# Performance work log

Hardware: AMD Instinct MI355X
Metric: run time of the kernel (lower is better)

The kernel has to match this reference:

```python
import jax, jax.numpy as jnp
import numpy as np

B, S, D = 4, 4096, 2048
E, H, SPE = 64, 1024, 1
NUM_SLOTS = E * SPE
TEMP = 1.0


def setup_inputs() -> dict:
    key = jax.random.key(0)
    ks = jax.random.split(key, 6)
    x = jax.random.normal(ks[0], (B, S, D), dtype=jnp.float32)
    W_disp = jax.random.normal(ks[1], (NUM_SLOTS, D), dtype=jnp.float32) * 0.02
    # torch Linear default init ~ U(-1/sqrt(fan_in), 1/sqrt(fan_in))
    W1 = jax.random.uniform(ks[2], (E, H, D), jnp.float32, -1.0, 1.0) / np.sqrt(D)
    b1 = jax.random.uniform(ks[3], (E, H), jnp.float32, -1.0, 1.0) / np.sqrt(D)
    W2 = jax.random.uniform(ks[4], (E, D, H), jnp.float32, -1.0, 1.0) / np.sqrt(H)
    b2 = jax.random.uniform(ks[5], (E, D), jnp.float32, -1.0, 1.0) / np.sqrt(H)
    return {"x": x, "W_disp": W_disp, "W1": W1, "b1": b1, "W2": W2, "b2": b2}


def reference(x, W_disp, W1, b1, W2, b2):
    # eval mode: dropout inactive, no calibration, z_loss_weight=0
    Bb, Ss, Dd = x.shape
    xf = x.reshape(-1, Dd)                       # (T, D)
    logits = (xf @ W_disp.T) / TEMP              # (T, num_slots)
    dispatch = jax.nn.softmax(logits, axis=0)    # softmax over tokens (T > 1)
    combine = jax.nn.softmax(logits, axis=-1)    # softmax over slots
    slot_inputs = dispatch.T @ xf                # (num_slots, D)
    x_exp = slot_inputs.reshape(E, SPE, Dd)      # (E, S_per, D)
    h = jnp.einsum('esd,ehd->esh', x_exp, W1) + b1[:, None, :]
    h = jax.nn.gelu(h, approximate=False)        # torch F.gelu is exact (erf)
    out = jnp.einsum('esh,edh->esd', h, W2) + b2[:, None, :]
    slot_outputs = out.reshape(NUM_SLOTS, Dd)
    y = combine @ slot_outputs                   # (T, D)
    return y.reshape(Bb, Ss, Dd)
```

## Files before the change

kernel.cpp:

```cpp
#include <hip/hip_runtime.h>
#include <math.h>

#define T_TOK 16384
#define D_DIM 2048
#define NSLOT 64
#define H_DIM 1024
#define KSPLIT 8
#define KCH 256
#define TBLK 128

__global__ __launch_bounds__(256) void k_logits(const float* __restrict__ x,
                                                const float* __restrict__ Wd,
                                                float* __restrict__ plog) {
    __shared__ float xs[128][32];
    __shared__ float ws[64][32];
    const int tid = threadIdx.x;
    const int tblk = blockIdx.x * TBLK;
    const int koff = blockIdx.y * KCH;
    const int tq = tid >> 3;
    const int sg = tid & 7;
    float acc[4][8] = {};

    for (int kc = 0; kc < KCH; kc += 32) {
        __syncthreads();
        #pragma unroll
        for (int ii = 0; ii < 4; ++ii) {
            int fi = tid + ii * 256; int t = fi >> 3, c = fi & 7;
            *(float4*)&xs[t][(c ^ (t & 7)) << 2] =
                *(const float4*)&x[(size_t)(tblk + t) * D_DIM + koff + kc + c * 4];
        }
        #pragma unroll
        for (int ii = 0; ii < 2; ++ii) {
            int fi = tid + ii * 256; int s = fi >> 3, c = fi & 7;
            *(float4*)&ws[s][(c ^ (s & 7)) << 2] =
                *(const float4*)&Wd[(size_t)s * D_DIM + koff + kc + c * 4];
        }
        __syncthreads();
        #pragma unroll
        for (int c = 0; c < 8; ++c) {
            float4 wv[8];
            #pragma unroll
            for (int j = 0; j < 8; ++j)
                wv[j] = *(const float4*)&ws[sg + 8 * j][(c ^ sg) << 2];
            #pragma unroll
            for (int i = 0; i < 4; ++i) {
                float4 xv = *(const float4*)&xs[tq + 32 * i][(c ^ (tq & 7)) << 2];
                #pragma unroll
                for (int j = 0; j < 8; ++j)
                    acc[i][j] += xv.x * wv[j].x + xv.y * wv[j].y +
                                 xv.z * wv[j].z + xv.w * wv[j].w;
            }
        }
    }
    const size_t ksbase = (size_t)blockIdx.y * T_TOK;
    #pragma unroll
    for (int i = 0; i < 4; ++i)
        #pragma unroll
        for (int j = 0; j < 8; ++j)
            plog[(ksbase + tblk + tq + 32 * i) * NSLOT + sg + 8 * j] = acc[i][j];
}

__global__ __launch_bounds__(256) void k_lsum(const float* __restrict__ plog,
                                              float* __restrict__ elog,
                                              float* __restrict__ pz) {
    __shared__ float zsh[4][64];
    const int tid = threadIdx.x;
    const int s = tid & 63, rq = tid >> 6;
    const int j0 = blockIdx.x * 256;
    float zacc = 0.f;
    for (int i = 0; i < 64; ++i) {
        int r = j0 + rq * 64 + i;
        float v = 0.f;
        #pragma unroll
        for (int ks = 0; ks < KSPLIT; ++ks)
            v += plog[((size_t)ks * T_TOK + r) * NSLOT + s];
        float e = __expf(v);
        elog[(size_t)r * NSLOT + s] = e;
        zacc += e;
    }
    zsh[rq][s] = zacc;
    __syncthreads();
    if (tid < 64)
        pz[(size_t)blockIdx.x * NSLOT + tid] =
            zsh[0][tid] + zsh[1][tid] + zsh[2][tid] + zsh[3][tid];
}

__global__ void k_zred(const float* __restrict__ pz, float* __restrict__ invZ) {
    float z = 0.f;
    for (int b = 0; b < 64; ++b) z += pz[b * NSLOT + threadIdx.x];
    invZ[threadIdx.x] = 1.f / z;
}

__global__ __launch_bounds__(256) void k_slot(const float* __restrict__ x,
        const float* __restrict__ elog, float* __restrict__ partial) {
    __shared__ float xs[32][256];
    __shared__ float pls[32][64];
    const int tid = threadIdx.x;
    const int d0 = blockIdx.x * 256;
    const int tc0 = blockIdx.y * 256;
    const int dg = tid & 31, sgq = tid >> 5;
    float4 acc0[8] = {}, acc1[8] = {};

    for (int sub = 0; sub < 8; ++sub) {
        const int t0 = tc0 + sub * 32;
        __syncthreads();
        #pragma unroll
        for (int ii = 0; ii < 8; ++ii) {
            int fi = tid + ii * 256; int r = fi >> 6, c4 = fi & 63;
            *(float4*)&xs[r][c4 * 4] =
                *(const float4*)&x[(size_t)(t0 + r) * D_DIM + d0 + c4 * 4];
        }
        #pragma unroll
        for (int ii = 0; ii < 2; ++ii) {
            int fi = tid + ii * 256; int r = fi >> 4, s4 = fi & 15;
            *(float4*)&pls[r][s4 * 4] =
                *(const float4*)&elog[(size_t)(t0 + r) * NSLOT + s4 * 4];
        }
        __syncthreads();
        for (int t = 0; t < 32; ++t) {
            float4 xv0 = *(const float4*)&xs[t][dg * 4];
            float4 xv1 = *(const float4*)&xs[t][128 + dg * 4];
            #pragma unroll
            for (int i = 0; i < 8; ++i) {
                float p = pls[t][sgq * 8 + i];
                acc0[i].x += p * xv0.x; acc0[i].y += p * xv0.y;
                acc0[i].z += p * xv0.z; acc0[i].w += p * xv0.w;
                acc1[i].x += p * xv1.x; acc1[i].y += p * xv1.y;
                acc1[i].z += p * xv1.z; acc1[i].w += p * xv1.w;
            }
        }
    }
    #pragma unroll
    for (int i = 0; i < 8; ++i) {
        int s = sgq * 8 + i;
        *(float4*)&partial[((size_t)blockIdx.y * NSLOT + s) * D_DIM + d0 + dg * 4] = acc0[i];
        *(float4*)&partial[((size_t)blockIdx.y * NSLOT + s) * D_DIM + d0 + 128 + dg * 4] = acc1[i];
    }
}

__global__ __launch_bounds__(256) void k_sred(const float* __restrict__ partial,
                                              const float* __restrict__ invZ,
                                              float* __restrict__ slot_in) {
    const size_t idx = (size_t)blockIdx.x * 256 + threadIdx.x;
    const float iz = invZ[idx >> 9];
    float4 a = {0.f, 0.f, 0.f, 0.f};
    for (int c = 0; c < 64; ++c) {
        float4 v = ((const float4*)partial)[(size_t)c * (NSLOT * D_DIM / 4) + idx];
        a.x += v.x; a.y += v.y; a.z += v.z; a.w += v.w;
    }
    a.x *= iz; a.y *= iz; a.z *= iz; a.w *= iz;
    ((float4*)slot_in)[idx] = a;
}

__global__ __launch_bounds__(256) void k_mlp1(const float* __restrict__ W1,
                                              const float* __restrict__ b1,
                                              const float* __restrict__ slot_in,
                                              float* __restrict__ h) {
    const int wave = threadIdx.x >> 6, lane = threadIdx.x & 63;
    const int row = blockIdx.x * 4 + wave;
    const int e = row >> 10;
    const float* wr = W1 + (size_t)row * D_DIM;
    const float* xr = slot_in + (size_t)e * D_DIM;
    float acc = 0.f;
    #pragma unroll
    for (int i = 0; i < 8; ++i) {
        int k = (lane + i * 64) * 4;
        float4 w4 = *(const float4*)(wr + k);
        float4 x4 = *(const float4*)(xr + k);
        acc += w4.x * x4.x + w4.y * x4.y + w4.z * x4.z + w4.w * x4.w;
    }
    #pragma unroll
    for (int off = 32; off; off >>= 1) acc += __shfl_xor(acc, off);
    if (lane == 0) {
        float v = acc + b1[row];
        h[row] = 0.5f * v * (1.f + erff(v * 0.70710678118654752f));
    }
}

__global__ __launch_bounds__(256) void k_mlp2(const float* __restrict__ W2,
                                              const float* __restrict__ b2,
                                              const float* __restrict__ h,
                                              float* __restrict__ slot_out) {
    const int wave = threadIdx.x >> 6, lane = threadIdx.x & 63;
    const int row = blockIdx.x * 4 + wave;
    const int e = row >> 11;
    const float* wr = W2 + (size_t)row * H_DIM;
    const float* xr = h + (size_t)e * H_DIM;
    float acc = 0.f;
    #pragma unroll
    for (int i = 0; i < 4; ++i) {
        int k = (lane + i * 64) * 4;
        float4 w4 = *(const float4*)(wr + k);
        float4 x4 = *(const float4*)(xr + k);
        acc += w4.x * x4.x + w4.y * x4.y + w4.z * x4.z + w4.w * x4.w;
    }
    #pragma unroll
    for (int off = 32; off; off >>= 1) acc += __shfl_xor(acc, off);
    if (lane == 0) slot_out[row] = acc + b2[row];
}

__global__ __launch_bounds__(256) void k_combine(const float* __restrict__ elog,
                                                 const float* __restrict__ so,
                                                 float* __restrict__ y) {
    __shared__ float cl[128][68];
    __shared__ float sol[64][128];
    __shared__ float rinv[128];
    const int tid = threadIdx.x;
    const int d0 = blockIdx.x * 128;
    const int tb = blockIdx.y * 128;
    const int tq = tid >> 4;
    const int dgq = tid & 15;
    #pragma unroll
    for (int ii = 0; ii < 8; ++ii) {
        int fi = tid + ii * 256; int r = fi >> 4, s4 = fi & 15;
        *(float4*)&cl[r][s4 * 4] =
            *(const float4*)&elog[(size_t)(tb + r) * NSLOT + s4 * 4];
    }
    #pragma unroll
    for (int ii = 0; ii < 8; ++ii) {
        int fi = tid + ii * 256; int r = fi >> 5, c4 = fi & 31;
        *(float4*)&sol[r][c4 * 4] =
            *(const float4*)&so[(size_t)r * D_DIM + d0 + c4 * 4];
    }
    __syncthreads();
    if (tid < 128) {
        float zs = 0.f;
        #pragma unroll
        for (int q = 0; q < 16; ++q) {
            float4 v = *(const float4*)&cl[tid][q * 4];
            zs += v.x + v.y + v.z + v.w;
        }
        rinv[tid] = 1.f / zs;
    }
    __syncthreads();
    float4 acc0[8] = {}, acc1[8] = {};
    for (int s = 0; s < 64; ++s) {
        float4 sv0 = *(const float4*)&sol[s][dgq * 4];
        float4 sv1 = *(const float4*)&sol[s][64 + dgq * 4];
        #pragma unroll
        for (int i = 0; i < 8; ++i) {
            float cv = cl[tq + 16 * i][s];
            acc0[i].x += cv * sv0.x; acc0[i].y += cv * sv0.y;
            acc0[i].z += cv * sv0.z; acc0[i].w += cv * sv0.w;
            acc1[i].x += cv * sv1.x; acc1[i].y += cv * sv1.y;
            acc1[i].z += cv * sv1.z; acc1[i].w += cv * sv1.w;
        }
    }
    #pragma unroll
    for (int i = 0; i < 8; ++i) {
        float rz = rinv[tq + 16 * i];
        acc0[i].x *= rz; acc0[i].y *= rz; acc0[i].z *= rz; acc0[i].w *= rz;
        acc1[i].x *= rz; acc1[i].y *= rz; acc1[i].z *= rz; acc1[i].w *= rz;
        *(float4*)&y[(size_t)(tb + tq + 16 * i) * D_DIM + d0 + dgq * 4] = acc0[i];
        *(float4*)&y[(size_t)(tb + tq + 16 * i) * D_DIM + d0 + 64 + dgq * 4] = acc1[i];
    }
}

extern "C" void kernel_launch(void* const* d_in, const int* in_sizes, int n_in,
                              void* d_out, int out_size, void* d_ws, size_t ws_size,
                              hipStream_t stream) {
    const float* x  = (const float*)d_in[0];
    const float* Wd = (const float*)d_in[1];
    const float* W1 = (const float*)d_in[2];
    const float* b1 = (const float*)d_in[3];
    const float* W2 = (const float*)d_in[4];
    const float* b2 = (const float*)d_in[5];
    float* y = (float*)d_out;

    float* w = (float*)d_ws;
    float* plog     = w;
    float* elog     = plog + (size_t)KSPLIT * T_TOK * NSLOT;
    float* pz       = elog + (size_t)T_TOK * NSLOT;
    float* invZ     = pz + 64 * NSLOT;
    float* partial  = invZ + NSLOT;
    float* slot_in  = partial + (size_t)64 * NSLOT * D_DIM;
    float* h        = slot_in + (size_t)NSLOT * D_DIM;
    float* slot_out = h + (size_t)NSLOT * H_DIM;

    k_logits<<<dim3(T_TOK / TBLK, KSPLIT), 256, 0, stream>>>(x, Wd, plog);
    k_lsum<<<64, 256, 0, stream>>>(plog, elog, pz);
    k_zred<<<1, 64, 0, stream>>>(pz, invZ);
    k_slot<<<dim3(8, 64), 256, 0, stream>>>(x, elog, partial);
    k_sred<<<128, 256, 0, stream>>>(partial, invZ, slot_in);
    k_mlp1<<<(NSLOT * H_DIM) / 4, 256, 0, stream>>>(W1, b1, slot_in, h);
    k_mlp2<<<(NSLOT * D_DIM) / 4, 256, 0, stream>>>(W2, b2, h, slot_out);
    k_combine<<<dim3(16, 128), 256, 0, stream>>>(elog, slot_out, y);
}
```

Measured before the change: 470.2 us.

## Spread logit-sum over more blocks, fold Z reduction into atomics, batch sred loads

k_lsum now runs on 512 blocks of 32 tokens each instead of 64 blocks of 256, which gives more parallelism to the memory-bound pass over plog. Per-slot partition sums are accumulated with atomicAdd into four striped buffers that k_logits zeroes, so the k_zred launch goes away and k_sred computes the reciprocal itself. k_sred also issues eight independent float4 loads per step to raise memory-level parallelism. In exchange, the float atomics make the summation order nondeterministic.

```diff
diff --git a/kernel.cpp b/kernel.cpp
--- a/kernel.cpp
+++ b/kernel.cpp
@@ -11,10 +11,12 @@
 
 __global__ __launch_bounds__(256) void k_logits(const float* __restrict__ x,
                                                 const float* __restrict__ Wd,
-                                                float* __restrict__ plog) {
+                                                float* __restrict__ plog,
+                                                float* __restrict__ pz4) {
     __shared__ float xs[128][32];
     __shared__ float ws[64][32];
     const int tid = threadIdx.x;
+    if (blockIdx.x == 0 && blockIdx.y == 0) pz4[tid] = 0.f;
     const int tblk = blockIdx.x * TBLK;
     const int koff = blockIdx.y * KCH;
     const int tq = tid >> 3;
@@ -62,14 +64,15 @@
 
 __global__ __launch_bounds__(256) void k_lsum(const float* __restrict__ plog,
                                               float* __restrict__ elog,
-                                              float* __restrict__ pz) {
+                                              float* __restrict__ pz4) {
     __shared__ float zsh[4][64];
     const int tid = threadIdx.x;
     const int s = tid & 63, rq = tid >> 6;
-    const int j0 = blockIdx.x * 256;
+    const int j0 = blockIdx.x * 32;
     float zacc = 0.f;
-    for (int i = 0; i < 64; ++i) {
-        int r = j0 + rq * 64 + i;
+    #pragma unroll
+    for (int i = 0; i < 8; ++i) {
+        int r = j0 + rq * 8 + i;
         float v = 0.f;
         #pragma unroll
         for (int ks = 0; ks < KSPLIT; ++ks)
@@ -81,14 +84,8 @@
     zsh[rq][s] = zacc;
     __syncthreads();
     if (tid < 64)
-        pz[(size_t)blockIdx.x * NSLOT + tid] =
-            zsh[0][tid] + zsh[1][tid] + zsh[2][tid] + zsh[3][tid];
-}
-
-__global__ void k_zred(const float* __restrict__ pz, float* __restrict__ invZ) {
-    float z = 0.f;
-    for (int b = 0; b < 64; ++b) z += pz[b * NSLOT + threadIdx.x];
-    invZ[threadIdx.x] = 1.f / z;
+        atomicAdd(&pz4[(blockIdx.x & 3) * 64 + tid],
+                  zsh[0][tid] + zsh[1][tid] + zsh[2][tid] + zsh[3][tid]);
 }
 
 __global__ __launch_bounds__(256) void k_slot(const float* __restrict__ x,
@@ -139,14 +136,22 @@
 }
 
 __global__ __launch_bounds__(256) void k_sred(const float* __restrict__ partial,
-                                              const float* __restrict__ invZ,
+                                              const float* __restrict__ pz4,
                                               float* __restrict__ slot_in) {
     const size_t idx = (size_t)blockIdx.x * 256 + threadIdx.x;
-    const float iz = invZ[idx >> 9];
+    const int s = (int)(idx >> 9);
+    const float iz = 1.f / (pz4[s] + pz4[64 + s] + pz4[128 + s] + pz4[192 + s]);
+    const float4* p4 = (const float4*)partial;
     float4 a = {0.f, 0.f, 0.f, 0.f};
-    for (int c = 0; c < 64; ++c) {
-        float4 v = ((const float4*)partial)[(size_t)c * (NSLOT * D_DIM / 4) + idx];
-        a.x += v.x; a.y += v.y; a.z += v.z; a.w += v.w;
+    for (int c0 = 0; c0 < 8; ++c0) {
+        float4 v[8];
+        #pragma unroll
+        for (int j = 0; j < 8; ++j)
+            v[j] = p4[(size_t)(c0 * 8 + j) * (NSLOT * D_DIM / 4) + idx];
+        #pragma unroll
+        for (int j = 0; j < 8; ++j) {
+            a.x += v[j].x; a.y += v[j].y; a.z += v[j].z; a.w += v[j].w;
+        }
     }
     a.x *= iz; a.y *= iz; a.z *= iz; a.w *= iz;
     ((float4*)slot_in)[idx] = a;
@@ -270,18 +275,16 @@
     float* w = (float*)d_ws;
     float* plog     = w;
     float* elog     = plog + (size_t)KSPLIT * T_TOK * NSLOT;
-    float* pz       = elog + (size_t)T_TOK * NSLOT;
-    float* invZ     = pz + 64 * NSLOT;
-    float* partial  = invZ + NSLOT;
+    float* pz4      = elog + (size_t)T_TOK * NSLOT;
+    float* partial  = pz4 + 256;
     float* slot_in  = partial + (size_t)64 * NSLOT * D_DIM;
     float* h        = slot_in + (size_t)NSLOT * D_DIM;
     float* slot_out = h + (size_t)NSLOT * H_DIM;
 
-    k_logits<<<dim3(T_TOK / TBLK, KSPLIT), 256, 0, stream>>>(x, Wd, plog);
-    k_lsum<<<64, 256, 0, stream>>>(plog, elog, pz);
-    k_zred<<<1, 64, 0, stream>>>(pz, invZ);
+    k_logits<<<dim3(T_TOK / TBLK, KSPLIT), 256, 0, stream>>>(x, Wd, plog, pz4);
+    k_lsum<<<512, 256, 0, stream>>>(plog, elog, pz4);
     k_slot<<<dim3(8, 64), 256, 0, stream>>>(x, elog, partial);
-    k_sred<<<128, 256, 0, stream>>>(partial, invZ, slot_in);
+    k_sred<<<128, 256, 0, stream>>>(partial, pz4, slot_in);
     k_mlp1<<<(NSLOT * H_DIM) / 4, 256, 0, stream>>>(W1, b1, slot_in, h);
     k_mlp2<<<(NSLOT * D_DIM) / 4, 256, 0, stream>>>(W2, b2, h, slot_out);
     k_combine<<<dim3(16, 128), 256, 0, stream>>>(elog, slot_out, y);
```

Result: faster. 446.9 us (-5.0%).
